# Optimization experiments

Hardware: AMD Instinct MI355X
Metric: run time of the kernel (lower is better)

The kernel has to match this reference:

```python
import jax, jax.numpy as jnp
import numpy as np

B, S, E, H = 4, 2048, 1024, 16
HD = E // H  # 64 head dim


def setup_inputs() -> dict:
    key = jax.random.key(0)
    ks = jax.random.split(key, 6)
    x = jax.random.normal(ks[0], (B, S, E), dtype=jnp.float32)
    mask = jax.random.randint(ks[1], (B, S, S), 0, 2, dtype=jnp.int32)
    # per-head qkv Linear(E -> 3*HD), stacked over heads: weight [H, 3*HD, E]
    lim = 1.0 / np.sqrt(E)
    Wqkv = jax.random.uniform(ks[2], (H, 3 * HD, E), minval=-lim, maxval=lim, dtype=jnp.float32)
    bqkv = jax.random.uniform(ks[3], (H, 3 * HD), minval=-lim, maxval=lim, dtype=jnp.float32)
    Wo = jax.random.uniform(ks[4], (E, E), minval=-lim, maxval=lim, dtype=jnp.float32)
    bo = jax.random.uniform(ks[5], (E,), minval=-lim, maxval=lim, dtype=jnp.float32)
    return {"x": x, "mask": mask, "Wqkv": Wqkv, "bqkv": bqkv, "Wo": Wo, "bo": bo}


def reference(x, mask, Wqkv, bqkv, Wo, bo):
    # fused per-head qkv projection: [B,S,E] x [H,3HD,E] -> [B,H,S,3HD]
    qkv = jnp.einsum('bse,hfe->bhsf', x, Wqkv) + bqkv[None, :, None, :]
    q, k, v = jnp.split(qkv, 3, axis=-1)  # each [B,H,S,HD]
    scale = 1.0 / jnp.sqrt(jnp.float32(HD))
    scores = jnp.einsum('bhqd,bhkd->bhqk', q, k) * scale  # [B,H,S,S]
    # NOTE: original masked_fill sets masked scores to 0.0 (not -inf)
    scores = jnp.where(mask[:, None, :, :] == 1, 0.0, scores)
    attn = jax.nn.softmax(scores, axis=-1)
    ctx = jnp.einsum('bhqk,bhkd->bhqd', attn, v)  # [B,H,S,HD]
    ctx = ctx.transpose(0, 2, 1, 3).reshape(B, S, E)  # concat heads
    return ctx @ Wo.T + bo
```

## Files before the change

kernel.cpp:

```cpp
#include <hip/hip_runtime.h>
#include <stdint.h>

#define B_ 4
#define S_ 2048
#define E_ 1024
#define H_ 16
#define HD_ 64

typedef __attribute__((ext_vector_type(8))) short bf16x8;
typedef __attribute__((ext_vector_type(4))) float f32x4;

__device__ __forceinline__ ushort f2b(float f) {
    union { float f; uint32_t u; } c; c.f = f;
    return (ushort)((c.u + 0x8000u) >> 16);
}

__device__ __forceinline__ uint32_t pkbf(float a, float b) {
    union { float f; uint32_t u; } ca, cb; ca.f = a; cb.f = b;
#if __has_builtin(__builtin_amdgcn_perm)
    return __builtin_amdgcn_perm(cb.u + 0x8000u, ca.u + 0x8000u, 0x07060302u);
#else
    return (uint32_t)f2b(a) | ((uint32_t)f2b(b) << 16);
#endif
}

#if __has_builtin(__builtin_amdgcn_exp2f)
#define EXP2(x) __builtin_amdgcn_exp2f(x)
#else
#define EXP2(x) exp2f(x)
#endif

__device__ __forceinline__ void gl2lds16(const ushort* g, const ushort* l) {
    __builtin_amdgcn_global_load_lds(
        (const __attribute__((address_space(1))) unsigned int*)g,
        (__attribute__((address_space(3))) unsigned int*)l,
        16, 0, 0);
}

__global__ __launch_bounds__(256) void cvt_all(
    const float* __restrict__ x, const float* __restrict__ wq, const float* __restrict__ wo,
    ushort* __restrict__ xb, ushort* __restrict__ wqb, ushort* __restrict__ wob) {
    int i = blockIdx.x * 256 + threadIdx.x;
    const float* src; ushort* dst; int off;
    if (i < 2097152)      { src = x;  dst = xb;  off = i; }
    else if (i < 2883584) { src = wq; dst = wqb; off = i - 2097152; }
    else                  { src = wo; dst = wob; off = i - 2883584; }
    float4 f = ((const float4*)src)[off];
    ushort4 o;
    o.x = f2b(f.x); o.y = f2b(f.y); o.z = f2b(f.z); o.w = f2b(f.w);
    ((ushort4*)dst)[off] = o;
}

__global__ __launch_bounds__(256) void pack_mask(const int* __restrict__ mask,
                                                 uint32_t* __restrict__ mb) {
    int i = blockIdx.x * 256 + threadIdx.x;
    unsigned long long bal = __ballot(mask[i] == 1);
    int lane = threadIdx.x & 63;
    if (lane < 2) {
        int b = i >> 22, q = (i >> 11) & 2047, c = i & 2047;
        int kt = c >> 6;
        mb[((uint64_t)(b * 32 + kt) * 2048 + q) * 2 + lane] =
            (lane == 0) ? (uint32_t)bal : (uint32_t)(bal >> 32);
    }
}

template <int KD>
__device__ __forceinline__ void gemm_bt_core(
    const ushort* __restrict__ A, const ushort* __restrict__ Bm,
    int m0, int n0, ushort* As, ushort* Bs, f32x4 (&acc)[4][4])
{
    const int tid  = threadIdx.x;
    const int lane = tid & 63;
    const int wave = tid >> 6;
    const int wm = wave >> 1, wn = wave & 1;
    const int fr = lane & 15;
    const int fk = (lane >> 4) * 8;
    const int lrow = lane >> 2;
    const int lk   = (lane & 3) * 8;

    const f32x4 fz = {0.f, 0.f, 0.f, 0.f};
#pragma unroll
    for (int i = 0; i < 4; ++i)
#pragma unroll
        for (int j = 0; j < 4; ++j) acc[i][j] = fz;

    for (int kt = 0; kt < KD / 32; ++kt) {
        const int k0 = kt * 32;
        __syncthreads();
#pragma unroll
        for (int t = 0; t < 2; ++t) {
            const int r0 = t * 64 + wave * 16;
            gl2lds16(&A [(uint64_t)(m0 + r0 + lrow) * KD + k0 + lk], &As[r0 * 32]);
            gl2lds16(&Bm[(uint64_t)(n0 + r0 + lrow) * KD + k0 + lk], &Bs[r0 * 32]);
        }
        __syncthreads();
        bf16x8 af[4], bfr[4];
#pragma unroll
        for (int i = 0; i < 4; ++i)
            af[i] = *(const bf16x8*)&As[(wm * 64 + i * 16 + fr) * 32 + fk];
#pragma unroll
        for (int j = 0; j < 4; ++j)
            bfr[j] = *(const bf16x8*)&Bs[(wn * 64 + j * 16 + fr) * 32 + fk];
#pragma unroll
        for (int i = 0; i < 4; ++i)
#pragma unroll
            for (int j = 0; j < 4; ++j)
                acc[i][j] = __builtin_amdgcn_mfma_f32_16x16x32_bf16(af[i], bfr[j], acc[i][j], 0, 0, 0);
    }
}

__global__ __launch_bounds__(256) void qkv_gemm(
    const ushort* __restrict__ xb, const ushort* __restrict__ wb,
    const float* __restrict__ bqkv,
    ushort* __restrict__ qo, ushort* __restrict__ ko, ushort* __restrict__ vto)
{
    __shared__ ushort As[128 * 32];
    __shared__ ushort Bs[128 * 32];
    f32x4 acc[4][4];
    const int m0 = blockIdx.x * 128;
    const int n0 = blockIdx.y * 128;
    gemm_bt_core<1024>(xb, wb, m0, n0, As, Bs, acc);

    const int lane = threadIdx.x & 63, wave = threadIdx.x >> 6;
    const int wm = wave >> 1, wn = wave & 1;
    const int col = lane & 15, rg = lane >> 4;
    const float QSC = 0.125f * 1.4426950408889634f;
#pragma unroll
    for (int j = 0; j < 4; ++j) {
        const int n = n0 + wn * 64 + j * 16 + col;
        const int h = n / 192, f = n % 192;
        const float bias = bqkv[n];
#pragma unroll
        for (int i2 = 0; i2 < 4; ++i2) {
            const int mbase = m0 + wm * 64 + i2 * 16 + rg * 4;
            if (f < 128) {
#pragma unroll
                for (int v = 0; v < 4; ++v) {
                    const int m = mbase + v;
                    const int b = m >> 11, s = m & 2047;
                    const float val = acc[i2][j][v] + bias;
                    if (f < 64) qo[((uint64_t)(b * 16 + h) * 2048 + s) * 64 + f]        = f2b(val * QSC);
                    else        ko[((uint64_t)(b * 16 + h) * 2048 + s) * 64 + (f - 64)] = f2b(val);
                }
            } else {
                const int b = mbase >> 11, s = mbase & 2047;
                ushort4 pk;
                pk.x = f2b(acc[i2][j][0] + bias);
                pk.y = f2b(acc[i2][j][1] + bias);
                pk.z = f2b(acc[i2][j][2] + bias);
                pk.w = f2b(acc[i2][j][3] + bias);
                *(ushort4*)&vto[((uint64_t)(b * 16 + h) * 64 + (f - 128)) * 2048 + s] = pk;
            }
        }
    }
}

__global__ __launch_bounds__(256, 3) void attn_kernel(
    const ushort* __restrict__ qa, const ushort* __restrict__ ka,
    const ushort* __restrict__ vta, const uint32_t* __restrict__ mbits,
    ushort* __restrict__ ctxo)
{
    __shared__ __align__(16) ushort LDSH[24576];
    ushort* const Ks0 = LDSH;
    ushort* const Vt0 = LDSH + 4096;
    ushort* const Ks1 = LDSH + 8192;
    ushort* const Vt1 = LDSH + 12288;
    ushort* const Ks2 = LDSH + 16384;
    ushort* const Vt2 = LDSH + 20480;
    ushort* const CTX = LDSH;

    const int bid = blockIdx.x;
    const int bh = (bid & 7) * 8 + (bid >> 7);
    const int qb = (bid >> 3) & 15;
    const int b = bh >> 4;
    const int tid = threadIdx.x, lane = tid & 63, wave = tid >> 6;
    const int col = lane & 15, rg = lane >> 4;

    const uint64_t bhoff = (uint64_t)bh * (S_ * 64);
    const ushort* qp = qa + bhoff + (uint64_t)qb * 128 * 64;
    const ushort* kp = ka + bhoff;
    const ushort* vp = vta + bhoff;
    const uint32_t* mk0 = mbits + ((uint64_t)(b * 32) * 2048 + qb * 128 + wave * 32 + col) * 2;
    const uint32_t* mk1 = mk0 + 32;

    const int lr = lane >> 3;
    const int usw = (lane & 7) ^ lr;
    const int r0s = wave * 16 + lr;
    const int r1s = r0s + 8;
    const int sg0 = (r0s & 32) | ((r0s & 12) << 1) | ((r0s & 16) >> 2) | (r0s & 3);
    const int sg1 = (r1s & 32) | ((r1s & 12) << 1) | ((r1s & 16) >> 2) | (r1s & 3);
    const int kb0 = sg0 * 64 + usw * 8;
    const int kb1 = sg1 * 64 + usw * 8;
    const int vb0 = r0s * 2048 + usw * 8;
    const int vb1 = r1s * 2048 + usw * 8;
    const int ldst0 = wave * 1024;
    const int ldst1 = ldst0 + 512;

    bf16x8 aq[2][2];
#pragma unroll
    for (int i = 0; i < 2; ++i)
#pragma unroll
        for (int k2 = 0; k2 < 2; ++k2)
            aq[i][k2] = *(const bf16x8*)&qp[(wave * 32 + i * 16 + col) * 64 + k2 * 32 + rg * 8];

    gl2lds16(&kp[kb0], &Ks0[ldst0]);
    gl2lds16(&kp[kb1], &Ks0[ldst1]);
    gl2lds16(&vp[vb0], &Vt0[ldst0]);
    gl2lds16(&vp[vb1], &Vt0[ldst1]);
    uint2 m_cur0 = *(const uint2*)mk0;
    uint2 m_cur1 = *(const uint2*)mk1;
    gl2lds16(&kp[4096 + kb0], &Ks1[ldst0]);
    gl2lds16(&kp[4096 + kb1], &Ks1[ldst1]);
    gl2lds16(&vp[vb0 + 64], &Vt1[ldst0]);
    gl2lds16(&vp[vb1 + 64], &Vt1[ldst1]);
    uint2 m_nxt0 = *(const uint2*)(mk0 + 4096);
    uint2 m_nxt1 = *(const uint2*)(mk1 + 4096);
    uint2 m_new0 = m_nxt0, m_new1 = m_nxt1;
    asm volatile("s_waitcnt vmcnt(0)" ::: "memory");
    __builtin_amdgcn_s_barrier();
    __builtin_amdgcn_sched_barrier(0);

    const f32x4 fz = {0.f, 0.f, 0.f, 0.f};
    f32x4 acc[4][2];
#pragma unroll
    for (int dt = 0; dt < 4; ++dt)
#pragma unroll
        for (int i = 0; i < 2; ++i) acc[dt][i] = fz;
    f32x4 acc5[2] = {fz, fz};

    bf16x8 vone;
#pragma unroll
    for (int e = 0; e < 8; ++e) vone[e] = (short)0x3F80;

    uint32_t bsel[2][4];
#pragma unroll
    for (int p = 0; p < 2; ++p)
#pragma unroll
        for (int v = 0; v < 4; ++v) bsel[p][v] = 1u << (rg * 8 + p * 4 + v);

    const int u0 = (rg ^ (col & 7)) << 3;

    const ushort* cK = Ks0; const ushort* cV = Vt0;
    const ushort* nK = Ks1; const ushort* nV = Vt1;
    ushort* tK = Ks2; ushort* tV = Vt2;

    for (int kt = 0; kt < 32; ++kt) {
        if (kt < 30) {
            const int k2 = (kt + 2) * 4096;
            gl2lds16(&kp[k2 + kb0], &tK[ldst0]);
            gl2lds16(&kp[k2 + kb1], &tK[ldst1]);
            gl2lds16(&vp[vb0 + (kt + 2) * 64], &tV[ldst0]);
            gl2lds16(&vp[vb1 + (kt + 2) * 64], &tV[ldst1]);
            m_new0 = *(const uint2*)(mk0 + (uint64_t)(kt + 2) * 4096);
            m_new1 = *(const uint2*)(mk1 + (uint64_t)(kt + 2) * 4096);
        }

        f32x4 sc[2][4];
        __builtin_amdgcn_s_setprio(1);
#pragma unroll
        for (int j = 0; j < 4; ++j) {
            bf16x8 bk0 = *(const bf16x8*)&cK[(j * 16 + col) * 64 + u0];
            bf16x8 bk1 = *(const bf16x8*)&cK[(j * 16 + col) * 64 + (u0 ^ 32)];
#pragma unroll
            for (int i = 0; i < 2; ++i) {
                f32x4 z = __builtin_amdgcn_mfma_f32_16x16x32_bf16(bk0, aq[i][0], fz, 0, 0, 0);
                sc[i][j] = __builtin_amdgcn_mfma_f32_16x16x32_bf16(bk1, aq[i][1], z, 0, 0, 0);
            }
        }
        __builtin_amdgcn_s_setprio(0);

        bf16x8 bp[2][2];
#pragma unroll
        for (int i = 0; i < 2; ++i) {
            const uint2 mw = i ? m_cur1 : m_cur0;
            union { uint32_t w[4]; bf16x8 v; } p0, p1;
#pragma unroll
            for (int j = 0; j < 4; ++j) {
                const uint32_t w = (j & 2) ? mw.y : mw.x;
                const int p = j & 1;
                float pe[4];
#pragma unroll
                for (int v = 0; v < 4; ++v) {
                    const float s = (w & bsel[p][v]) ? 0.f : sc[i][j][v];
                    pe[v] = EXP2(s);
                }
                const uint32_t lo = pkbf(pe[0], pe[1]);
                const uint32_t hi = pkbf(pe[2], pe[3]);
                if (j < 2) { p0.w[p * 2] = lo; p0.w[p * 2 + 1] = hi; }
                else       { p1.w[p * 2] = lo; p1.w[p * 2 + 1] = hi; }
            }
            bp[i][0] = p0.v;
            bp[i][1] = p1.v;
        }

        __builtin_amdgcn_s_setprio(1);
#pragma unroll
        for (int i = 0; i < 2; ++i) {
            acc5[i] = __builtin_amdgcn_mfma_f32_16x16x32_bf16(vone, bp[i][0], acc5[i], 0, 0, 0);
            acc5[i] = __builtin_amdgcn_mfma_f32_16x16x32_bf16(vone, bp[i][1], acc5[i], 0, 0, 0);
        }
#pragma unroll
        for (int dt = 0; dt < 4; ++dt) {
            bf16x8 av0 = *(const bf16x8*)&cV[(dt * 16 + col) * 64 + u0];
            bf16x8 av1 = *(const bf16x8*)&cV[(dt * 16 + col) * 64 + (u0 ^ 32)];
#pragma unroll
            for (int i = 0; i < 2; ++i) {
                acc[dt][i] = __builtin_amdgcn_mfma_f32_16x16x32_bf16(av0, bp[i][0], acc[dt][i], 0, 0, 0);
                acc[dt][i] = __builtin_amdgcn_mfma_f32_16x16x32_bf16(av1, bp[i][1], acc[dt][i], 0, 0, 0);
            }
        }
        __builtin_amdgcn_s_setprio(0);

        if (kt < 30) {
            asm volatile("s_waitcnt vmcnt(6)" ::: "memory");
        } else {
            asm volatile("s_waitcnt vmcnt(0)" ::: "memory");
        }
        __builtin_amdgcn_s_barrier();
        __builtin_amdgcn_sched_barrier(0);

        const ushort* oK = cK; const ushort* oV = cV;
        cK = nK; cV = nV; nK = tK; nV = tV; tK = (ushort*)oK; tV = (ushort*)oV;
        m_cur0 = m_nxt0; m_cur1 = m_nxt1; m_nxt0 = m_new0; m_nxt1 = m_new1;
    }

    float linv[2];
#pragma unroll
    for (int i = 0; i < 2; ++i) linv[i] = 1.0f / acc5[i][0];

#pragma unroll
    for (int dt = 0; dt < 4; ++dt)
#pragma unroll
        for (int i = 0; i < 2; ++i) {
            const int q = wave * 32 + i * 16 + col;
            const int d = dt * 16 + rg * 4;
            const int gg = (d >> 3) ^ (q & 7);
            ushort4 pk;
            pk.x = f2b(acc[dt][i][0] * linv[i]);
            pk.y = f2b(acc[dt][i][1] * linv[i]);
            pk.z = f2b(acc[dt][i][2] * linv[i]);
            pk.w = f2b(acc[dt][i][3] * linv[i]);
            *(ushort4*)&CTX[q * 64 + gg * 8 + (d & 7)] = pk;
        }
    __syncthreads();
    const int h = bh & 15;
    const uint64_t obase = (uint64_t)(b * S_ + qb * 128) * E_ + (uint64_t)h * 64;
#pragma unroll
    for (int t4 = 0; t4 < 4; ++t4) {
        const int id = tid + t4 * 256;
        const int r = id >> 3, c8 = id & 7;
        *(bf16x8*)&ctxo[obase + (uint64_t)r * E_ + c8 * 8] =
            *(const bf16x8*)&CTX[r * 64 + ((c8 ^ (r & 7)) << 3)];
    }
}

__global__ __launch_bounds__(256) void out_gemm(
    const ushort* __restrict__ ctxb, const ushort* __restrict__ wob,
    const float* __restrict__ bo, float* __restrict__ out)
{
    __shared__ ushort As[128 * 32];
    __shared__ ushort Bs[128 * 32];
    f32x4 acc[4][4];
    const int m0 = blockIdx.x * 128;
    const int n0 = blockIdx.y * 128;
    gemm_bt_core<1024>(ctxb, wob, m0, n0, As, Bs, acc);

    const int lane = threadIdx.x & 63, wave = threadIdx.x >> 6;
    const int wm = wave >> 1, wn = wave & 1;
    const int col = lane & 15, rg = lane >> 4;
#pragma unroll
    for (int j = 0; j < 4; ++j) {
        const int n = n0 + wn * 64 + j * 16 + col;
        const float bias = bo[n];
#pragma unroll
        for (int i2 = 0; i2 < 4; ++i2) {
            const int mb2 = m0 + wm * 64 + i2 * 16 + rg * 4;
#pragma unroll
            for (int v = 0; v < 4; ++v)
                out[(uint64_t)(mb2 + v) * 1024 + n] = acc[i2][j][v] + bias;
        }
    }
}

extern "C" void kernel_launch(void* const* d_in, const int* in_sizes, int n_in,
                              void* d_out, int out_size, void* d_ws, size_t ws_size,
                              hipStream_t stream)
{
    const float* x    = (const float*)d_in[0];
    const int*   mask = (const int*)d_in[1];
    const float* Wqkv = (const float*)d_in[2];
    const float* bqkv = (const float*)d_in[3];
    const float* Wo   = (const float*)d_in[4];
    const float* bo   = (const float*)d_in[5];
    float* out = (float*)d_out;

    char* p = (char*)d_ws;
    ushort* xb  = (ushort*)p; p += (size_t)8388608 * 2;
    ushort* wqb = (ushort*)p; p += (size_t)3145728 * 2;
    ushort* wob = (ushort*)p; p += (size_t)1048576 * 2;
    ushort* qo  = (ushort*)p; p += (size_t)8388608 * 2;
    ushort* ko  = (ushort*)p; p += (size_t)8388608 * 2;
    ushort* vto = (ushort*)p; p += (size_t)8388608 * 2;
    ushort* ctx = (ushort*)p; p += (size_t)8388608 * 2;
    uint32_t* mb = (uint32_t*)p;

    cvt_all<<<12288, 256, 0, stream>>>(x, Wqkv, Wo, xb, wqb, wob);
    pack_mask<<<65536, 256, 0, stream>>>(mask, mb);
    qkv_gemm<<<dim3(64, 24), 256, 0, stream>>>(xb, wqb, bqkv, qo, ko, vto);
    attn_kernel<<<1024, 256, 0, stream>>>(qo, ko, vto, mb, ctx);
    out_gemm<<<dim3(64, 8), 256, 0, stream>>>(ctx, wob, bo, out);
}
```

Baseline: 361.0 us.

## Triple-buffer GEMM LDS staging and swizzle block order for L2 locality

The shared bf16 GEMM core now prefetches two k-tiles ahead into a three-slot LDS ring. It replaces the double __syncthreads per step with a vmcnt wait and a single barrier, and raises wave priority around the MFMA block. Both GEMM kernels switch to a 1D grid with a swizzled block-to-tile mapping so that concurrently running blocks share operand rows in cache. This aims to hide global-load latency in the QKV and output projections, at the cost of 48KB of LDS per block, which may reduce occupancy.

```diff
diff --git a/kernel.cpp b/kernel.cpp
--- a/kernel.cpp
+++ b/kernel.cpp
@@ -67,8 +67,9 @@
 template <int KD>
 __device__ __forceinline__ void gemm_bt_core(
     const ushort* __restrict__ A, const ushort* __restrict__ Bm,
-    int m0, int n0, ushort* As, ushort* Bs, f32x4 (&acc)[4][4])
+    int m0, int n0, ushort* L, f32x4 (&acc)[4][4])
 {
+    constexpr int NST = KD / 32;
     const int tid  = threadIdx.x;
     const int lane = tid & 63;
     const int wave = tid >> 6;
@@ -84,29 +85,60 @@
 #pragma unroll
         for (int j = 0; j < 4; ++j) acc[i][j] = fz;
 
-    for (int kt = 0; kt < KD / 32; ++kt) {
-        const int k0 = kt * 32;
-        __syncthreads();
-#pragma unroll
-        for (int t = 0; t < 2; ++t) {
-            const int r0 = t * 64 + wave * 16;
-            gl2lds16(&A [(uint64_t)(m0 + r0 + lrow) * KD + k0 + lk], &As[r0 * 32]);
-            gl2lds16(&Bm[(uint64_t)(n0 + r0 + lrow) * KD + k0 + lk], &Bs[r0 * 32]);
-        }
-        __syncthreads();
+    ushort* s0 = L;
+    ushort* s1 = L + 8192;
+    ushort* s2 = L + 16384;
+
+    const uint64_t arow = (uint64_t)(m0 + lrow) * KD + lk;
+    const uint64_t brow = (uint64_t)(n0 + lrow) * KD + lk;
+
+#define GEMM_STAGE(k0, slot)                                                     \
+    {                                                                            \
+        _Pragma("unroll")                                                        \
+        for (int t = 0; t < 2; ++t) {                                            \
+            const int r0 = t * 64 + wave * 16;                                   \
+            gl2lds16(&A [arow + (uint64_t)r0 * KD + (k0)], &(slot)[r0 * 32]);    \
+            gl2lds16(&Bm[brow + (uint64_t)r0 * KD + (k0)], &(slot)[4096 + r0 * 32]); \
+        }                                                                        \
+    }
+
+    GEMM_STAGE(0, s0);
+    GEMM_STAGE(32, s1);
+    asm volatile("s_waitcnt vmcnt(4)" ::: "memory");
+    __builtin_amdgcn_s_barrier();
+    __builtin_amdgcn_sched_barrier(0);
+
+    ushort* cur = s0; ushort* nxt = s1; ushort* tgt = s2;
+
+    for (int kt = 0; kt < NST; ++kt) {
+        if (kt < NST - 2) GEMM_STAGE((kt + 2) * 32, tgt);
+
         bf16x8 af[4], bfr[4];
 #pragma unroll
         for (int i = 0; i < 4; ++i)
-            af[i] = *(const bf16x8*)&As[(wm * 64 + i * 16 + fr) * 32 + fk];
+            af[i] = *(const bf16x8*)&cur[(wm * 64 + i * 16 + fr) * 32 + fk];
 #pragma unroll
         for (int j = 0; j < 4; ++j)
-            bfr[j] = *(const bf16x8*)&Bs[(wn * 64 + j * 16 + fr) * 32 + fk];
+            bfr[j] = *(const bf16x8*)&cur[4096 + (wn * 64 + j * 16 + fr) * 32 + fk];
+        __builtin_amdgcn_s_setprio(1);
 #pragma unroll
         for (int i = 0; i < 4; ++i)
 #pragma unroll
             for (int j = 0; j < 4; ++j)
                 acc[i][j] = __builtin_amdgcn_mfma_f32_16x16x32_bf16(af[i], bfr[j], acc[i][j], 0, 0, 0);
-    }
+        __builtin_amdgcn_s_setprio(0);
+
+        if (kt < NST - 2) {
+            asm volatile("s_waitcnt vmcnt(4)" ::: "memory");
+        } else {
+            asm volatile("s_waitcnt vmcnt(0)" ::: "memory");
+        }
+        __builtin_amdgcn_s_barrier();
+        __builtin_amdgcn_sched_barrier(0);
+
+        ushort* o = cur; cur = nxt; nxt = tgt; tgt = o;
+    }
+#undef GEMM_STAGE
 }
 
 __global__ __launch_bounds__(256) void qkv_gemm(
@@ -114,12 +146,13 @@
     const float* __restrict__ bqkv,
     ushort* __restrict__ qo, ushort* __restrict__ ko, ushort* __restrict__ vto)
 {
-    __shared__ ushort As[128 * 32];
-    __shared__ ushort Bs[128 * 32];
+    __shared__ __align__(16) ushort L[24576];
     f32x4 acc[4][4];
-    const int m0 = blockIdx.x * 128;
-    const int n0 = blockIdx.y * 128;
-    gemm_bt_core<1024>(xb, wb, m0, n0, As, Bs, acc);
+    const int lin = blockIdx.x;
+    const int swz = (lin & 7) * 192 + (lin >> 3);
+    const int m0 = (swz & 63) * 128;
+    const int n0 = (swz >> 6) * 128;
+    gemm_bt_core<1024>(xb, wb, m0, n0, L, acc);
 
     const int lane = threadIdx.x & 63, wave = threadIdx.x >> 6;
     const int wm = wave >> 1, wn = wave & 1;
@@ -358,12 +391,13 @@
     const ushort* __restrict__ ctxb, const ushort* __restrict__ wob,
     const float* __restrict__ bo, float* __restrict__ out)
 {
-    __shared__ ushort As[128 * 32];
-    __shared__ ushort Bs[128 * 32];
+    __shared__ __align__(16) ushort L[24576];
     f32x4 acc[4][4];
-    const int m0 = blockIdx.x * 128;
-    const int n0 = blockIdx.y * 128;
-    gemm_bt_core<1024>(ctxb, wob, m0, n0, As, Bs, acc);
+    const int lin = blockIdx.x;
+    const int swz = (lin & 7) * 64 + (lin >> 3);
+    const int m0 = (swz & 63) * 128;
+    const int n0 = (swz >> 6) * 128;
+    gemm_bt_core<1024>(ctxb, wob, m0, n0, L, acc);
 
     const int lane = threadIdx.x & 63, wave = threadIdx.x >> 6;
     const int wm = wave >> 1, wn = wave & 1;
@@ -406,7 +440,7 @@
 
     cvt_all<<<12288, 256, 0, stream>>>(x, Wqkv, Wo, xb, wqb, wob);
     pack_mask<<<65536, 256, 0, stream>>>(mask, mb);
-    qkv_gemm<<<dim3(64, 24), 256, 0, stream>>>(xb, wqb, bqkv, qo, ko, vto);
+    qkv_gemm<<<1536, 256, 0, stream>>>(xb, wqb, bqkv, qo, ko, vto);
     attn_kernel<<<1024, 256, 0, stream>>>(qo, ko, vto, mb, ctx);
-    out_gemm<<<dim3(64, 8), 256, 0, stream>>>(ctx, wob, bo, out);
-}
+    out_gemm<<<512, 256, 0, stream>>>(ctx, wob, bo, out);
+}
```

Result: no change. 359.3 us (-0.5%).
